# Optimization experiments

Hardware: AMD Instinct MI355X
Metric: run time of the kernel (lower is better)

## Reference

```python
import jax, jax.numpy as jnp
import numpy as np

B, N = 16, 4096
N_IN, E_OUT = 128, 128          # inpt_dim[1], outp_dim[0]
OUT_N = 128                     # outp_dim[1]
G_DIM, CTXT_DIM = 64, 64
NODE_IN = E_OUT + N_IN          # 256, pre_ln size
CTXT_IN = G_DIM + CTXT_DIM      # 128
HID_F, HID_A = 256, 128
N_HEADS = 4
HEAD_DIM = OUT_N // N_HEADS     # 32
LN_EPS = 1e-5


def _init_w(key, fan_in, fan_out):
    return jax.random.normal(key, (fan_in, fan_out), jnp.float32) / np.float32(np.sqrt(fan_in))


def setup_inputs() -> dict:
    key = jax.random.key(0)
    ks = jax.random.split(key, 10)
    nodes = jax.random.normal(ks[0], (B, N, N_IN), jnp.float32)
    pooled_edges = jax.random.normal(ks[1], (B, N, E_OUT), jnp.float32)
    # variable-length graphs: valid prefix per graph (at least half the nodes)
    lengths = jax.random.randint(ks[2], (B,), N // 2, N + 1)
    mask = jnp.arange(N)[None, :] < lengths[:, None]
    globs = jax.random.normal(ks[3], (B, G_DIM), jnp.float32)
    ctxt = jax.random.normal(ks[4], (B, CTXT_DIM), jnp.float32)
    return {
        "nodes": nodes,
        "pooled_edges": pooled_edges,
        "mask": mask,
        "globs": globs,
        "ctxt": ctxt,
        "ln_g": jnp.ones((NODE_IN,), jnp.float32),
        "ln_b": jnp.zeros((NODE_IN,), jnp.float32),
        "feat_w1": _init_w(ks[5], NODE_IN + CTXT_IN, HID_F),
        "feat_b1": jnp.zeros((HID_F,), jnp.float32),
        "feat_w2": _init_w(ks[6], HID_F, OUT_N),
        "feat_b2": jnp.zeros((OUT_N,), jnp.float32),
        "attn_w1": _init_w(ks[7], NODE_IN + CTXT_IN, HID_A),
        "attn_b1": jnp.zeros((HID_A,), jnp.float32),
        "attn_w2": _init_w(ks[8], HID_A, N_HEADS),
        "attn_b2": jnp.zeros((N_HEADS,), jnp.float32),
    }


def _mlp(x, w1, b1, w2, b2):
    # DenseNetwork: one hidden block with LeakyReLU ("lrlu"), linear output
    h = jax.nn.leaky_relu(x @ w1 + b1)
    return h @ w2 + b2


def reference(nodes, pooled_edges, mask, globs, ctxt, ln_g, ln_b,
              feat_w1, feat_b1, feat_w2, feat_b2,
              attn_w1, attn_b1, attn_w2, attn_b2):
    # nodes = cat([graph.nodes, pooled_edges]) -> pre-LayerNorm
    x = jnp.concatenate([nodes, pooled_edges], axis=-1)           # [B,N,256]
    mu = jnp.mean(x, axis=-1, keepdims=True)
    var = jnp.var(x, axis=-1, keepdims=True)
    x = (x - mu) * jax.lax.rsqrt(var + LN_EPS) * ln_g + ln_b

    # high-level context broadcast to every node
    hl = jnp.concatenate([globs, ctxt], axis=-1)                   # [B,128]
    hl = jnp.broadcast_to(hl[:, None, :], (x.shape[0], x.shape[1], hl.shape[-1]))
    xin = jnp.concatenate([x, hl], axis=-1)                        # [B,N,384]

    # attention net with -inf padding, softmax over node axis (dim=-2)
    logits = _mlp(xin, attn_w1, attn_b1, attn_w2, attn_b2)          # [B,N,H]
    logits = jnp.where(mask[..., None], logits, -jnp.inf)
    w = jax.nn.softmax(logits, axis=1) / np.float32(np.sqrt(OUT_N))
    w = jnp.where(mask[..., None], w, 0.0)

    # feature net with 0 padding + residual (same_size)
    feats = _mlp(xin, feat_w1, feat_b1, feat_w2, feat_b2)           # [B,N,128]
    feats = jnp.where(mask[..., None], feats, 0.0)
    new_nodes = feats + nodes

    # expand per-head weights across head_dim, flatten, weighted node pooling
    w_full = jnp.repeat(w, HEAD_DIM, axis=-1)                       # [B,N,128]
    pooled = jnp.sum(new_nodes * w_full, axis=1)                    # [B,128]
    return (new_nodes, pooled)
```

## Files before the change

### kernel.cpp

```cpp
#include <hip/hip_runtime.h>
#include <stdint.h>

typedef unsigned short u16;
typedef unsigned char  u8;
typedef unsigned int   u32;
typedef __attribute__((ext_vector_type(8))) short bf16x8;
typedef __attribute__((ext_vector_type(4))) float f32x4;

static __device__ __forceinline__ float bf2f(u32 u) {
    union { u32 i; float f; } x; x.i = u << 16; return x.f;
}
static __device__ __forceinline__ u16 f2bf(float f) {
    union { u32 i; float f; } x; x.f = f;
    return (u16)((x.i + 0x7fffu + ((x.i >> 16) & 1u)) >> 16);
}
static __device__ __forceinline__ u32 packbf(float a, float b) {
    return (u32)f2bf(a) | ((u32)f2bf(b) << 16);
}
static __device__ __forceinline__ float ldf(const void* p, int i, int isf32) {
    return isf32 ? ((const float*)p)[i] : bf2f(((const u16*)p)[i]);
}
static __device__ __forceinline__ bool mvalid(const void* mask, int g, int mi32) {
    return mi32 ? (((const int*)mask)[g] != 0) : (((const u8*)mask)[g] != 0);
}

#define NTOT 65536
#define SXLD 264
#define SHLD 136
#define BM   64

__global__ __launch_bounds__(256) void k0_prep(
    const void* __restrict__ feat_w1, const void* __restrict__ attn_w1,
    const void* __restrict__ feat_b1, const void* __restrict__ attn_b1,
    const void* __restrict__ feat_w2, const void* __restrict__ attn_w2,
    const void* __restrict__ globs, const void* __restrict__ ctxt,
    const void* __restrict__ ln_g,
    u16* __restrict__ W1t, u16* __restrict__ W2t, u16* __restrict__ aw2t,
    float* __restrict__ hlc)
{
    __shared__ u16 tile[64][66];
    __shared__ float hl[128];
    const int isf32 = (((const u32*)ln_g)[0] == 0x3F800000u);
    const int bid = blockIdx.x;
    const int t = threadIdx.x;

    if (bid < 24) {
        int jt = bid >> 2, kt = bid & 3;
        int j0 = jt * 64, k0 = kt * 64;
        int jj = t & 63, kq = t >> 6;
#pragma unroll
        for (int r = 0; r < 16; r++) {
            int kk = r * 4 + kq;
            int j = j0 + jj;
            float v = (j < 256) ? ldf(feat_w1, (k0 + kk) * 256 + j, isf32)
                                : ldf(attn_w1, (k0 + kk) * 128 + (j - 256), isf32);
            tile[kk][jj] = f2bf(v);
        }
        __syncthreads();
        int kk2 = t & 63, jq = t >> 6;
#pragma unroll
        for (int r = 0; r < 16; r++) {
            int jj2 = r * 4 + jq;
            W1t[(size_t)(j0 + jj2) * 256 + k0 + kk2] = tile[kk2][jj2];
        }
    } else if (bid < 32) {
        int id2 = bid - 24;
        int ct2 = id2 >> 2, kt = id2 & 3;
        int c0 = ct2 * 64, k0 = kt * 64;
        int cc = t & 63, kq = t >> 6;
#pragma unroll
        for (int r = 0; r < 16; r++) {
            int kk = r * 4 + kq;
            tile[kk][cc] = f2bf(ldf(feat_w2, (k0 + kk) * 128 + c0 + cc, isf32));
        }
        __syncthreads();
        int kk2 = t & 63, cq = t >> 6;
#pragma unroll
        for (int r = 0; r < 16; r++) {
            int cc2 = r * 4 + cq;
            W2t[(size_t)(c0 + cc2) * 256 + k0 + kk2] = tile[kk2][cc2];
        }
    } else if (bid == 32) {
#pragma unroll
        for (int i = 0; i < 8; i++) {
            int e = i * 256 + t;
            int n = e >> 7, k = e & 127;
            aw2t[e] = (n < 4) ? f2bf(ldf(attn_w2, k * 4 + n, isf32)) : (u16)0;
        }
    } else {
        int b = bid - 33;
        if (t < 64)       hl[t] = ldf(globs, b * 64 + t, isf32);
        else if (t < 128) hl[t] = ldf(ctxt, b * 64 + (t - 64), isf32);
        __syncthreads();
        {
            float s = ldf(feat_b1, t, isf32);
#pragma unroll 8
            for (int c = 0; c < 128; c++)
                s += hl[c] * ldf(feat_w1, (256 + c) * 256 + t, isf32);
            hlc[b * 384 + t] = s;
        }
        if (t < 128) {
            float s = ldf(attn_b1, t, isf32);
#pragma unroll 8
            for (int c = 0; c < 128; c++)
                s += hl[c] * ldf(attn_w1, (256 + c) * 128 + t, isf32);
            hlc[b * 384 + 256 + t] = s;
        }
    }
}

__global__ __launch_bounds__(256, 3) void k_mega(
    const void* __restrict__ nodes, const void* __restrict__ edges,
    const void* __restrict__ ln_g, const void* __restrict__ ln_b,
    const u16* __restrict__ W1t, const u16* __restrict__ W2t,
    const u16* __restrict__ aw2t, const float* __restrict__ hlc,
    const void* __restrict__ attn_b2, const void* __restrict__ feat_b2,
    const void* __restrict__ mask,
    float* __restrict__ logits, void* __restrict__ outp)
{
    __shared__ __align__(16) u16 sX[BM * SXLD];
    __shared__ __align__(16) u16 sH[BM * SHLD];
    __shared__ float sG[256], sBt[256];
    const int t = threadIdx.x;
    const int g0 = blockIdx.x * BM;
    const int b = g0 >> 12;
    const int isf32 = (((const u32*)ln_g)[0] == 0x3F800000u);
    const int mi32  = (((const u32*)mask)[0] == 1u);

    sG[t]  = ldf(ln_g, t, isf32);
    sBt[t] = ldf(ln_b, t, isf32);
    __syncthreads();

#pragma unroll
    for (int half = 0; half < 2; half++) {
        const int r = half * 32 + (t >> 3), q8 = t & 7;
        u32 pk[16];
#pragma unroll
        for (int j = 0; j < 4; j++) {
            int c = q8 + j * 8;
            if (isf32) {
                const float* src = (c < 16)
                    ? ((const float*)nodes + (size_t)(g0 + r) * 128 + c * 8)
                    : ((const float*)edges + (size_t)(g0 + r) * 128 + (c - 16) * 8);
                float4 v0 = ((const float4*)src)[0];
                float4 v1 = ((const float4*)src)[1];
                pk[4 * j]     = packbf(v0.x, v0.y);
                pk[4 * j + 1] = packbf(v0.z, v0.w);
                pk[4 * j + 2] = packbf(v1.x, v1.y);
                pk[4 * j + 3] = packbf(v1.z, v1.w);
            } else {
                const u16* src = (c < 16)
                    ? ((const u16*)nodes + (size_t)(g0 + r) * 128 + c * 8)
                    : ((const u16*)edges + (size_t)(g0 + r) * 128 + (c - 16) * 8);
                uint4 v = ((const uint4*)src)[0];
                pk[4 * j] = v.x; pk[4 * j + 1] = v.y;
                pk[4 * j + 2] = v.z; pk[4 * j + 3] = v.w;
            }
        }
        float s = 0.f, q = 0.f;
#pragma unroll
        for (int i = 0; i < 16; i++) {
            float lo = bf2f(pk[i] & 0xffffu), hi = bf2f(pk[i] >> 16);
            s += lo + hi; q += lo * lo + hi * hi;
        }
        s += __shfl_xor(s, 1, 64); s += __shfl_xor(s, 2, 64); s += __shfl_xor(s, 4, 64);
        q += __shfl_xor(q, 1, 64); q += __shfl_xor(q, 2, 64); q += __shfl_xor(q, 4, 64);
        float mu = s * (1.f / 256.f);
        float var = q * (1.f / 256.f) - mu * mu;
        float rs = rsqrtf(var + 1e-5f);
#pragma unroll
        for (int j = 0; j < 4; j++) {
            int c = q8 + j * 8;
            u32 ow[4];
#pragma unroll
            for (int k2 = 0; k2 < 4; k2++) {
                int col = c * 8 + k2 * 2;
                u32 w2 = pk[4 * j + k2];
                float y0 = (bf2f(w2 & 0xffffu) - mu) * rs * sG[col]     + sBt[col];
                float y1 = (bf2f(w2 >> 16)     - mu) * rs * sG[col + 1] + sBt[col + 1];
                ow[k2] = packbf(y0, y1);
            }
            *(uint4*)&sX[r * SXLD + c * 8] = make_uint4(ow[0], ow[1], ow[2], ow[3]);
        }
    }
    __syncthreads();

    const int w = t >> 6, l = t & 63;
    const int lr = l & 15, lq = l >> 4;

    f32x4 acc2[4][2];
#pragma unroll
    for (int rt = 0; rt < 4; rt++)
#pragma unroll
        for (int ct = 0; ct < 2; ct++) acc2[rt][ct] = (f32x4){0.f, 0.f, 0.f, 0.f};

    const int order[3] = {2, 0, 1};
#pragma unroll
    for (int oi = 0; oi < 3; oi++) {
        const int nt = order[oi];

        float hbv[2];
#pragma unroll
        for (int ct = 0; ct < 2; ct++)
            hbv[ct] = hlc[b * 384 + nt * 128 + w * 32 + ct * 16 + lr];

        f32x4 acc1[4][2];
#pragma unroll
        for (int rt = 0; rt < 4; rt++)
#pragma unroll
            for (int ct = 0; ct < 2; ct++) acc1[rt][ct] = (f32x4){0.f, 0.f, 0.f, 0.f};

        const u16* Wp = W1t + (size_t)(nt * 128 + w * 32 + lr) * 256;
#pragma unroll
        for (int kh = 0; kh < 2; kh++) {
            bf16x8 bW[4][2];
#pragma unroll
            for (int kk = 0; kk < 4; kk++)
#pragma unroll
                for (int ct = 0; ct < 2; ct++)
                    bW[kk][ct] = *(const bf16x8*)(Wp + ct * 16 * 256 + (kh * 4 + kk) * 32 + lq * 8);
#pragma unroll
            for (int kk = 0; kk < 4; kk++) {
                bf16x8 aF[4];
#pragma unroll
                for (int rt = 0; rt < 4; rt++)
                    aF[rt] = *(const bf16x8*)&sX[(rt * 16 + lr) * SXLD + ((kh * 4 + kk) * 4 + lq) * 8];
#pragma unroll
                for (int rt = 0; rt < 4; rt++)
#pragma unroll
                    for (int ct = 0; ct < 2; ct++)
                        acc1[rt][ct] = __builtin_amdgcn_mfma_f32_16x16x32_bf16(aF[rt], bW[kk][ct], acc1[rt][ct], 0, 0, 0);
            }
        }

        __syncthreads();
#pragma unroll
        for (int rt = 0; rt < 4; rt++)
#pragma unroll
            for (int ct = 0; ct < 2; ct++)
#pragma unroll
                for (int reg = 0; reg < 4; reg++) {
                    int row = rt * 16 + lq * 4 + reg;
                    int col = w * 32 + ct * 16 + lr;
                    float hv = acc1[rt][ct][reg] + hbv[ct];
                    hv = (hv >= 0.f) ? hv : 0.01f * hv;
                    sH[row * SHLD + col] = f2bf(hv);
                }
        __syncthreads();

        if (nt == 2) {
            f32x4 accL = (f32x4){0.f, 0.f, 0.f, 0.f};
#pragma unroll
            for (int kk = 0; kk < 4; kk++) {
                bf16x8 aF = *(const bf16x8*)&sH[(w * 16 + lr) * SHLD + (kk * 4 + lq) * 8];
                bf16x8 bF = *(const bf16x8*)(aw2t + lr * 128 + kk * 32 + lq * 8);
                accL = __builtin_amdgcn_mfma_f32_16x16x32_bf16(aF, bF, accL, 0, 0, 0);
            }
            if (lr < 4) {
                float bias = ldf(attn_b2, lr, isf32);
#pragma unroll
                for (int reg = 0; reg < 4; reg++) {
                    int row = g0 + w * 16 + lq * 4 + reg;
                    logits[(size_t)lr * NTOT + row] = accL[reg] + bias;
                }
            }
        } else {
            const u16* W2p = W2t + (size_t)(w * 32 + lr) * 256 + nt * 128;
            bf16x8 bW2[4][2];
#pragma unroll
            for (int kk = 0; kk < 4; kk++)
#pragma unroll
                for (int ct = 0; ct < 2; ct++)
                    bW2[kk][ct] = *(const bf16x8*)(W2p + ct * 16 * 256 + kk * 32 + lq * 8);
#pragma unroll
            for (int kk = 0; kk < 4; kk++) {
                bf16x8 aF[4];
#pragma unroll
                for (int rt = 0; rt < 4; rt++)
                    aF[rt] = *(const bf16x8*)&sH[(rt * 16 + lr) * SHLD + (kk * 4 + lq) * 8];
#pragma unroll
                for (int rt = 0; rt < 4; rt++)
#pragma unroll
                    for (int ct = 0; ct < 2; ct++)
                        acc2[rt][ct] = __builtin_amdgcn_mfma_f32_16x16x32_bf16(aF[rt], bW2[kk][ct], acc2[rt][ct], 0, 0, 0);
            }
        }
    }

#pragma unroll
    for (int rt = 0; rt < 4; rt++)
#pragma unroll
        for (int ct = 0; ct < 2; ct++)
#pragma unroll
            for (int reg = 0; reg < 4; reg++) {
                int row = rt * 16 + lq * 4 + reg;
                int col = w * 32 + ct * 16 + lr;
                int g = g0 + row;
                float v = acc2[rt][ct][reg] + ldf(feat_b2, col, isf32);
                v = mvalid(mask, g, mi32) ? v : 0.f;
                v += ldf(nodes, g * 128 + col, isf32);
                size_t idx = (size_t)g * 128 + col;
                if (isf32) ((float*)outp)[idx] = v;
                else       ((u16*)outp)[idx] = f2bf(v);
            }
}

__global__ __launch_bounds__(1024) void k_softmax(
    const float* __restrict__ logits, const void* __restrict__ mask,
    const void* __restrict__ ln_g,
    float* __restrict__ wbuf, float* __restrict__ pooled)
{
    __shared__ float red[32];
    const int bh = blockIdx.x;
    const int b = bh >> 2, h = bh & 3;
    const int t = threadIdx.x;
    const int mi32 = (((const u32*)mask)[0] == 1u);
    if (t < 32) pooled[bh * 32 + t] = 0.f;

    float4 lg = ((const float4*)(logits + (size_t)h * NTOT + b * 4096))[t];
    int v0, v1, v2, v3;
    if (mi32) {
        int4 m4 = ((const int4*)mask)[b * 1024 + t];
        v0 = m4.x; v1 = m4.y; v2 = m4.z; v3 = m4.w;
    } else {
        u32 mb = ((const u32*)mask)[b * 1024 + t];
        v0 = mb & 255; v1 = (mb >> 8) & 255; v2 = (mb >> 16) & 255; v3 = mb >> 24;
    }
    float mx = -1e30f;
    if (v0) mx = lg.x;
    if (v1) mx = fmaxf(mx, lg.y);
    if (v2) mx = fmaxf(mx, lg.z);
    if (v3) mx = fmaxf(mx, lg.w);
#pragma unroll
    for (int o = 1; o < 64; o <<= 1) mx = fmaxf(mx, __shfl_xor(mx, o, 64));
    if ((t & 63) == 0) red[t >> 6] = mx;
    __syncthreads();
    float m2 = red[0];
#pragma unroll
    for (int i = 1; i < 16; i++) m2 = fmaxf(m2, red[i]);
    float e0 = v0 ? expf(lg.x - m2) : 0.f;
    float e1 = v1 ? expf(lg.y - m2) : 0.f;
    float e2 = v2 ? expf(lg.z - m2) : 0.f;
    float e3 = v3 ? expf(lg.w - m2) : 0.f;
    float sv = e0 + e1 + e2 + e3;
#pragma unroll
    for (int o = 1; o < 64; o <<= 1) sv += __shfl_xor(sv, o, 64);
    __syncthreads();
    if ((t & 63) == 0) red[16 + (t >> 6)] = sv;
    __syncthreads();
    float s2 = 0.f;
#pragma unroll
    for (int i = 0; i < 16; i++) s2 += red[16 + i];
    float inv = 0.08838834764831845f / s2;
    float4 o4 = make_float4(e0 * inv, e1 * inv, e2 * inv, e3 * inv);
    ((float4*)(wbuf + (size_t)h * NTOT + b * 4096))[t] = o4;
}

__global__ __launch_bounds__(256) void k_pool(
    const void* __restrict__ outp, const float* __restrict__ wbuf,
    const void* __restrict__ ln_g, float* __restrict__ pooled)
{
    __shared__ float sW[4][32];
    __shared__ float pacc[8][128];
    const int blk = blockIdx.x;
    const int b = blk >> 7, s = blk & 127;
    const int t = threadIdx.x;
    const int isf32 = (((const u32*)ln_g)[0] == 0x3F800000u);

    if (t < 128) {
        int h = t >> 5, n = t & 31;
        sW[h][n] = wbuf[(size_t)h * NTOT + b * 4096 + s * 32 + n];
    }
    __syncthreads();

    const int c4 = (t & 31) * 4, r8 = t >> 5;
    const int h = c4 >> 5;
    const size_t rowbase = (size_t)(b * 4096 + s * 32);
    float a0 = 0.f, a1 = 0.f, a2 = 0.f, a3 = 0.f;
    if (isf32) {
        const float* op = (const float*)outp;
#pragma unroll
        for (int i = 0; i < 4; i++) {
            int row = i * 8 + r8;
            float4 v = *(const float4*)(op + (rowbase + row) * 128 + c4);
            float wv = sW[h][row];
            a0 += v.x * wv; a1 += v.y * wv; a2 += v.z * wv; a3 += v.w * wv;
        }
    } else {
        const u16* op = (const u16*)outp;
#pragma unroll
        for (int i = 0; i < 4; i++) {
            int row = i * 8 + r8;
            uint2 v = *(const uint2*)(op + (rowbase + row) * 128 + c4);
            float wv = sW[h][row];
            a0 += bf2f(v.x & 0xffffu) * wv; a1 += bf2f(v.x >> 16) * wv;
            a2 += bf2f(v.y & 0xffffu) * wv; a3 += bf2f(v.y >> 16) * wv;
        }
    }
    *(float4*)&pacc[r8][c4] = make_float4(a0, a1, a2, a3);
    __syncthreads();
    if (t < 128) {
        float sum = 0.f;
#pragma unroll
        for (int r = 0; r < 8; r++) sum += pacc[r][t];
        atomicAdd(&pooled[b * 128 + t], sum);
    }
}

__global__ __launch_bounds__(256) void k_fin(const float* __restrict__ pooled,
                                             const void* __restrict__ ln_g,
                                             void* __restrict__ outbase)
{
    int t = blockIdx.x * 256 + threadIdx.x;
    const int isf32 = (((const u32*)ln_g)[0] == 0x3F800000u);
    if (t < 2048) {
        size_t off = (size_t)NTOT * 128 + t;
        if (isf32) ((float*)outbase)[off] = pooled[t];
        else       ((u16*)outbase)[off] = f2bf(pooled[t]);
    }
}

extern "C" void kernel_launch(void* const* d_in, const int* in_sizes, int n_in,
                              void* d_out, int out_size, void* d_ws, size_t ws_size,
                              hipStream_t stream)
{
    const void* nodes   = d_in[0];
    const void* edges   = d_in[1];
    const void* mask    = d_in[2];
    const void* globs   = d_in[3];
    const void* ctxt    = d_in[4];
    const void* ln_g    = d_in[5];
    const void* ln_b    = d_in[6];
    const void* feat_w1 = d_in[7];
    const void* feat_b1 = d_in[8];
    const void* feat_w2 = d_in[9];
    const void* feat_b2 = d_in[10];
    const void* attn_w1 = d_in[11];
    const void* attn_b1 = d_in[12];
    const void* attn_w2 = d_in[13];
    const void* attn_b2 = d_in[14];

    char* ws = (char*)d_ws;
    u16*   W1t    = (u16*)ws;   ws += (size_t)384 * 256 * 2;
    u16*   W2t    = (u16*)ws;   ws += (size_t)128 * 256 * 2;
    u16*   aw2t   = (u16*)ws;   ws += (size_t)16 * 128 * 2;
    float* hlc    = (float*)ws; ws += (size_t)16 * 384 * 4;
    float* logits = (float*)ws; ws += (size_t)NTOT * 4 * 4;
    float* wbuf   = (float*)ws; ws += (size_t)NTOT * 4 * 4;
    float* pooled = (float*)ws; ws += (size_t)2048 * 4;

    k0_prep  <<<dim3(49),   dim3(256),  0, stream>>>(feat_w1, attn_w1, feat_b1, attn_b1,
                                                     feat_w2, attn_w2, globs, ctxt, ln_g,
                                                     W1t, W2t, aw2t, hlc);
    k_mega   <<<dim3(1024), dim3(256),  0, stream>>>(nodes, edges, ln_g, ln_b, W1t, W2t,
                                                     aw2t, hlc, attn_b2, feat_b2, mask,
                                                     logits, d_out);
    k_softmax<<<dim3(64),   dim3(1024), 0, stream>>>(logits, mask, ln_g, wbuf, pooled);
    k_pool   <<<dim3(2048), dim3(256),  0, stream>>>(d_out, wbuf, ln_g, pooled);
    k_fin    <<<dim3(8),    dim3(256),  0, stream>>>(pooled, ln_g, d_out);
}
```

Before: 229.0 us.

## Split mega-kernel tile into two 32-row subtiles with prefetch and double-buffered sH

Each block now processes its 64 rows as two sequential 32-row subtiles instead of one 64-row tile. The global loads for both subtiles are issued up front so the second tile's input fetch overlaps the first tile's compute. The hidden-activation buffer is double-buffered, which removes one barrier per stage, and occupancy is raised from 3 to 4 blocks per CU through the smaller LDS footprint and fewer accumulators. In exchange, W1/W2 weight fragments are reloaded for each subtile, and the registers holding the prefetched data add pressure.

```diff
diff --git a/kernel.cpp b/kernel.cpp
--- a/kernel.cpp
+++ b/kernel.cpp
@@ -27,7 +27,10 @@
 #define NTOT 65536
 #define SXLD 264
 #define SHLD 136
-#define BM   64
+
+#define BAR() do { asm volatile("s_waitcnt lgkmcnt(0)" ::: "memory"); \
+                   __builtin_amdgcn_s_barrier();                      \
+                   asm volatile("" ::: "memory"); } while (0)
 
 __global__ __launch_bounds__(256) void k0_prep(
     const void* __restrict__ feat_w1, const void* __restrict__ attn_w1,
@@ -109,7 +112,7 @@
     }
 }
 
-__global__ __launch_bounds__(256, 3) void k_mega(
+__global__ __launch_bounds__(256, 4) void k_mega(
     const void* __restrict__ nodes, const void* __restrict__ edges,
     const void* __restrict__ ln_g, const void* __restrict__ ln_b,
     const u16* __restrict__ W1t, const u16* __restrict__ W2t,
@@ -118,45 +121,62 @@
     const void* __restrict__ mask,
     float* __restrict__ logits, void* __restrict__ outp)
 {
-    __shared__ __align__(16) u16 sX[BM * SXLD];
-    __shared__ __align__(16) u16 sH[BM * SHLD];
+    __shared__ __align__(16) u16 sX[32 * SXLD];
+    __shared__ __align__(16) u16 sH[2][32 * SHLD];
     __shared__ float sG[256], sBt[256];
     const int t = threadIdx.x;
-    const int g0 = blockIdx.x * BM;
-    const int b = g0 >> 12;
     const int isf32 = (((const u32*)ln_g)[0] == 0x3F800000u);
     const int mi32  = (((const u32*)mask)[0] == 1u);
+    const int r = t >> 3, q8 = t & 7;
+    const int g00 = blockIdx.x * 64;
+    const int g01 = g00 + 32;
 
     sG[t]  = ldf(ln_g, t, isf32);
     sBt[t] = ldf(ln_b, t, isf32);
-    __syncthreads();
-
-#pragma unroll
-    for (int half = 0; half < 2; half++) {
-        const int r = half * 32 + (t >> 3), q8 = t & 7;
-        u32 pk[16];
+
+    float4 f0a[4], f0b[4], f1a[4];
+    uint4  u0[4],  u1[4];
+    if (isf32) {
 #pragma unroll
         for (int j = 0; j < 4; j++) {
             int c = q8 + j * 8;
-            if (isf32) {
-                const float* src = (c < 16)
-                    ? ((const float*)nodes + (size_t)(g0 + r) * 128 + c * 8)
-                    : ((const float*)edges + (size_t)(g0 + r) * 128 + (c - 16) * 8);
-                float4 v0 = ((const float4*)src)[0];
-                float4 v1 = ((const float4*)src)[1];
-                pk[4 * j]     = packbf(v0.x, v0.y);
-                pk[4 * j + 1] = packbf(v0.z, v0.w);
-                pk[4 * j + 2] = packbf(v1.x, v1.y);
-                pk[4 * j + 3] = packbf(v1.z, v1.w);
-            } else {
-                const u16* src = (c < 16)
-                    ? ((const u16*)nodes + (size_t)(g0 + r) * 128 + c * 8)
-                    : ((const u16*)edges + (size_t)(g0 + r) * 128 + (c - 16) * 8);
-                uint4 v = ((const uint4*)src)[0];
-                pk[4 * j] = v.x; pk[4 * j + 1] = v.y;
-                pk[4 * j + 2] = v.z; pk[4 * j + 3] = v.w;
-            }
-        }
+            const float* s0 = (c < 16)
+                ? ((const float*)nodes + (size_t)(g00 + r) * 128 + c * 8)
+                : ((const float*)edges + (size_t)(g00 + r) * 128 + (c - 16) * 8);
+            f0a[j] = ((const float4*)s0)[0];
+            f0b[j] = ((const float4*)s0)[1];
+        }
+#pragma unroll
+        for (int j = 0; j < 4; j++) {
+            int c = q8 + j * 8;
+            const float* s1 = (c < 16)
+                ? ((const float*)nodes + (size_t)(g01 + r) * 128 + c * 8)
+                : ((const float*)edges + (size_t)(g01 + r) * 128 + (c - 16) * 8);
+            f1a[j] = ((const float4*)s1)[0];
+        }
+    } else {
+#pragma unroll
+        for (int j = 0; j < 4; j++) {
+            int c = q8 + j * 8;
+            const u16* s0 = (c < 16)
+                ? ((const u16*)nodes + (size_t)(g00 + r) * 128 + c * 8)
+                : ((const u16*)edges + (size_t)(g00 + r) * 128 + (c - 16) * 8);
+            u0[j] = ((const uint4*)s0)[0];
+        }
+#pragma unroll
+        for (int j = 0; j < 4; j++) {
+            int c = q8 + j * 8;
+            const u16* s1 = (c < 16)
+                ? ((const u16*)nodes + (size_t)(g01 + r) * 128 + c * 8)
+                : ((const u16*)edges + (size_t)(g01 + r) * 128 + (c - 16) * 8);
+            u1[j] = ((const uint4*)s1)[0];
+        }
+    }
+    BAR();
+
+    u32 pk[16];
+
+    auto ln_to_sX = [&]() {
         float s = 0.f, q = 0.f;
 #pragma unroll
         for (int i = 0; i < 16; i++) {
@@ -182,127 +202,176 @@
             }
             *(uint4*)&sX[r * SXLD + c * 8] = make_uint4(ow[0], ow[1], ow[2], ow[3]);
         }
-    }
-    __syncthreads();
+    };
+
+    if (isf32) {
+#pragma unroll
+        for (int j = 0; j < 4; j++) {
+            pk[4 * j]     = packbf(f0a[j].x, f0a[j].y);
+            pk[4 * j + 1] = packbf(f0a[j].z, f0a[j].w);
+            pk[4 * j + 2] = packbf(f0b[j].x, f0b[j].y);
+            pk[4 * j + 3] = packbf(f0b[j].z, f0b[j].w);
+        }
+    } else {
+#pragma unroll
+        for (int j = 0; j < 4; j++) {
+            pk[4 * j] = u0[j].x; pk[4 * j + 1] = u0[j].y;
+            pk[4 * j + 2] = u0[j].z; pk[4 * j + 3] = u0[j].w;
+        }
+    }
+    ln_to_sX();
+    BAR();
 
     const int w = t >> 6, l = t & 63;
     const int lr = l & 15, lq = l >> 4;
 
-    f32x4 acc2[4][2];
-#pragma unroll
-    for (int rt = 0; rt < 4; rt++)
-#pragma unroll
-        for (int ct = 0; ct < 2; ct++) acc2[rt][ct] = (f32x4){0.f, 0.f, 0.f, 0.f};
-
-    const int order[3] = {2, 0, 1};
-#pragma unroll
-    for (int oi = 0; oi < 3; oi++) {
-        const int nt = order[oi];
-
-        float hbv[2];
-#pragma unroll
-        for (int ct = 0; ct < 2; ct++)
-            hbv[ct] = hlc[b * 384 + nt * 128 + w * 32 + ct * 16 + lr];
-
-        f32x4 acc1[4][2];
-#pragma unroll
-        for (int rt = 0; rt < 4; rt++)
-#pragma unroll
-            for (int ct = 0; ct < 2; ct++) acc1[rt][ct] = (f32x4){0.f, 0.f, 0.f, 0.f};
-
-        const u16* Wp = W1t + (size_t)(nt * 128 + w * 32 + lr) * 256;
-#pragma unroll
-        for (int kh = 0; kh < 2; kh++) {
-            bf16x8 bW[4][2];
-#pragma unroll
-            for (int kk = 0; kk < 4; kk++)
+    auto do_tile = [&](int g0) {
+        const int b = g0 >> 12;
+        f32x4 acc2[2][2];
+#pragma unroll
+        for (int rt = 0; rt < 2; rt++)
+#pragma unroll
+            for (int ct = 0; ct < 2; ct++) acc2[rt][ct] = (f32x4){0.f, 0.f, 0.f, 0.f};
+
+        const int order[3] = {2, 0, 1};
+#pragma unroll
+        for (int oi = 0; oi < 3; oi++) {
+            const int nt = order[oi];
+            u16* sHc = &sH[oi & 1][0];
+
+            float hbv[2];
+#pragma unroll
+            for (int ct = 0; ct < 2; ct++)
+                hbv[ct] = hlc[b * 384 + nt * 128 + w * 32 + ct * 16 + lr];
+
+            f32x4 acc1[2][2];
+#pragma unroll
+            for (int rt = 0; rt < 2; rt++)
+#pragma unroll
+                for (int ct = 0; ct < 2; ct++) acc1[rt][ct] = (f32x4){0.f, 0.f, 0.f, 0.f};
+
+            const u16* Wp = W1t + (size_t)(nt * 128 + w * 32 + lr) * 256;
+#pragma unroll
+            for (int kh = 0; kh < 2; kh++) {
+                bf16x8 bW[4][2];
+#pragma unroll
+                for (int kk = 0; kk < 4; kk++)
+#pragma unroll
+                    for (int ct = 0; ct < 2; ct++)
+                        bW[kk][ct] = *(const bf16x8*)(Wp + ct * 16 * 256 + (kh * 4 + kk) * 32 + lq * 8);
+#pragma unroll
+                for (int kk = 0; kk < 4; kk++) {
+                    bf16x8 aF[2];
+#pragma unroll
+                    for (int rt = 0; rt < 2; rt++)
+                        aF[rt] = *(const bf16x8*)&sX[(rt * 16 + lr) * SXLD + ((kh * 4 + kk) * 4 + lq) * 8];
+#pragma unroll
+                    for (int rt = 0; rt < 2; rt++)
+#pragma unroll
+                        for (int ct = 0; ct < 2; ct++)
+                            acc1[rt][ct] = __builtin_amdgcn_mfma_f32_16x16x32_bf16(aF[rt], bW[kk][ct], acc1[rt][ct], 0, 0, 0);
+                }
+            }
+
+#pragma unroll
+            for (int rt = 0; rt < 2; rt++)
 #pragma unroll
                 for (int ct = 0; ct < 2; ct++)
-                    bW[kk][ct] = *(const bf16x8*)(Wp + ct * 16 * 256 + (kh * 4 + kk) * 32 + lq * 8);
-#pragma unroll
-            for (int kk = 0; kk < 4; kk++) {
-                bf16x8 aF[4];
-#pragma unroll
-                for (int rt = 0; rt < 4; rt++)
-                    aF[rt] = *(const bf16x8*)&sX[(rt * 16 + lr) * SXLD + ((kh * 4 + kk) * 4 + lq) * 8];
-#pragma unroll
-                for (int rt = 0; rt < 4; rt++)
+#pragma unroll
+                    for (int reg = 0; reg < 4; reg++) {
+                        int row = rt * 16 + lq * 4 + reg;
+                        int col = w * 32 + ct * 16 + lr;
+                        float hv = acc1[rt][ct][reg] + hbv[ct];
+                        hv = (hv >= 0.f) ? hv : 0.01f * hv;
+                        sHc[row * SHLD + col] = f2bf(hv);
+                    }
+            BAR();
+
+            if (nt == 2) {
+                if (w < 2) {
+                    f32x4 accL = (f32x4){0.f, 0.f, 0.f, 0.f};
+#pragma unroll
+                    for (int kk = 0; kk < 4; kk++) {
+                        bf16x8 aF = *(const bf16x8*)&sHc[(w * 16 + lr) * SHLD + (kk * 4 + lq) * 8];
+                        bf16x8 bF = *(const bf16x8*)(aw2t + lr * 128 + kk * 32 + lq * 8);
+                        accL = __builtin_amdgcn_mfma_f32_16x16x32_bf16(aF, bF, accL, 0, 0, 0);
+                    }
+                    if (lr < 4) {
+                        float bias = ldf(attn_b2, lr, isf32);
+#pragma unroll
+                        for (int reg = 0; reg < 4; reg++) {
+                            int row = g0 + w * 16 + lq * 4 + reg;
+                            logits[(size_t)lr * NTOT + row] = accL[reg] + bias;
+                        }
+                    }
+                }
+            } else {
+                const u16* W2p = W2t + (size_t)(w * 32 + lr) * 256 + nt * 128;
+                bf16x8 bW2[4][2];
+#pragma unroll
+                for (int kk = 0; kk < 4; kk++)
 #pragma unroll
                     for (int ct = 0; ct < 2; ct++)
-                        acc1[rt][ct] = __builtin_amdgcn_mfma_f32_16x16x32_bf16(aF[rt], bW[kk][ct], acc1[rt][ct], 0, 0, 0);
+                        bW2[kk][ct] = *(const bf16x8*)(W2p + ct * 16 * 256 + kk * 32 + lq * 8);
+#pragma unroll
+                for (int kk = 0; kk < 4; kk++) {
+                    bf16x8 aF[2];
+#pragma unroll
+                    for (int rt = 0; rt < 2; rt++)
+                        aF[rt] = *(const bf16x8*)&sHc[(rt * 16 + lr) * SHLD + (kk * 4 + lq) * 8];
+#pragma unroll
+                    for (int rt = 0; rt < 2; rt++)
+#pragma unroll
+                        for (int ct = 0; ct < 2; ct++)
+                            acc2[rt][ct] = __builtin_amdgcn_mfma_f32_16x16x32_bf16(aF[rt], bW2[kk][ct], acc2[rt][ct], 0, 0, 0);
+                }
             }
         }
 
-        __syncthreads();
-#pragma unroll
-        for (int rt = 0; rt < 4; rt++)
+#pragma unroll
+        for (int rt = 0; rt < 2; rt++)
 #pragma unroll
             for (int ct = 0; ct < 2; ct++)
 #pragma unroll
                 for (int reg = 0; reg < 4; reg++) {
                     int row = rt * 16 + lq * 4 + reg;
                     int col = w * 32 + ct * 16 + lr;
-                    float hv = acc1[rt][ct][reg] + hbv[ct];
-                    hv = (hv >= 0.f) ? hv : 0.01f * hv;
-                    sH[row * SHLD + col] = f2bf(hv);
+                    int g = g0 + row;
+                    float v = acc2[rt][ct][reg] + ldf(feat_b2, col, isf32);
+                    v = mvalid(mask, g, mi32) ? v : 0.f;
+                    v += ldf(nodes, g * 128 + col, isf32);
+                    size_t idx = (size_t)g * 128 + col;
+                    if (isf32) ((float*)outp)[idx] = v;
+                    else       ((u16*)outp)[idx] = f2bf(v);
                 }
-        __syncthreads();
-
-        if (nt == 2) {
-            f32x4 accL = (f32x4){0.f, 0.f, 0.f, 0.f};
-#pragma unroll
-            for (int kk = 0; kk < 4; kk++) {
-                bf16x8 aF = *(const bf16x8*)&sH[(w * 16 + lr) * SHLD + (kk * 4 + lq) * 8];
-                bf16x8 bF = *(const bf16x8*)(aw2t + lr * 128 + kk * 32 + lq * 8);
-                accL = __builtin_amdgcn_mfma_f32_16x16x32_bf16(aF, bF, accL, 0, 0, 0);
-            }
-            if (lr < 4) {
-                float bias = ldf(attn_b2, lr, isf32);
-#pragma unroll
-                for (int reg = 0; reg < 4; reg++) {
-                    int row = g0 + w * 16 + lq * 4 + reg;
-                    logits[(size_t)lr * NTOT + row] = accL[reg] + bias;
-                }
-            }
-        } else {
-            const u16* W2p = W2t + (size_t)(w * 32 + lr) * 256 + nt * 128;
-            bf16x8 bW2[4][2];
-#pragma unroll
-            for (int kk = 0; kk < 4; kk++)
-#pragma unroll
-                for (int ct = 0; ct < 2; ct++)
-                    bW2[kk][ct] = *(const bf16x8*)(W2p + ct * 16 * 256 + kk * 32 + lq * 8);
-#pragma unroll
-            for (int kk = 0; kk < 4; kk++) {
-                bf16x8 aF[4];
-#pragma unroll
-                for (int rt = 0; rt < 4; rt++)
-                    aF[rt] = *(const bf16x8*)&sH[(rt * 16 + lr) * SHLD + (kk * 4 + lq) * 8];
-#pragma unroll
-                for (int rt = 0; rt < 4; rt++)
-#pragma unroll
-                    for (int ct = 0; ct < 2; ct++)
-                        acc2[rt][ct] = __builtin_amdgcn_mfma_f32_16x16x32_bf16(aF[rt], bW2[kk][ct], acc2[rt][ct], 0, 0, 0);
-            }
-        }
-    }
-
-#pragma unroll
-    for (int rt = 0; rt < 4; rt++)
-#pragma unroll
-        for (int ct = 0; ct < 2; ct++)
-#pragma unroll
-            for (int reg = 0; reg < 4; reg++) {
-                int row = rt * 16 + lq * 4 + reg;
-                int col = w * 32 + ct * 16 + lr;
-                int g = g0 + row;
-                float v = acc2[rt][ct][reg] + ldf(feat_b2, col, isf32);
-                v = mvalid(mask, g, mi32) ? v : 0.f;
-                v += ldf(nodes, g * 128 + col, isf32);
-                size_t idx = (size_t)g * 128 + col;
-                if (isf32) ((float*)outp)[idx] = v;
-                else       ((u16*)outp)[idx] = f2bf(v);
-            }
+    };
+
+    do_tile(g00);
+
+    if (isf32) {
+#pragma unroll
+        for (int j = 0; j < 4; j++) {
+            int c = q8 + j * 8;
+            const float* s1 = (c < 16)
+                ? ((const float*)nodes + (size_t)(g01 + r) * 128 + c * 8)
+                : ((const float*)edges + (size_t)(g01 + r) * 128 + (c - 16) * 8);
+            float4 fb = ((const float4*)s1)[1];
+            pk[4 * j]     = packbf(f1a[j].x, f1a[j].y);
+            pk[4 * j + 1] = packbf(f1a[j].z, f1a[j].w);
+            pk[4 * j + 2] = packbf(fb.x, fb.y);
+            pk[4 * j + 3] = packbf(fb.z, fb.w);
+        }
+    } else {
+#pragma unroll
+        for (int j = 0; j < 4; j++) {
+            pk[4 * j] = u1[j].x; pk[4 * j + 1] = u1[j].y;
+            pk[4 * j + 2] = u1[j].z; pk[4 * j + 3] = u1[j].w;
+        }
+    }
+    ln_to_sX();
+    BAR();
+
+    do_tile(g01);
 }
 
 __global__ __launch_bounds__(1024) void k_softmax(
```

Result: slower. 242.1 us (+5.7%).

## Fuse softmax and weighted pooling into main kernel via per-block online-softmax partials

Applied to the files above, without the earlier changes.

Each 64-row block now computes its local max and exp-sum of the attention logits and its exp-weighted partial pooled sums while the output tile is still in registers. It writes only a small per-block record, and a single small final kernel rescales and combines the records. This removes the logits and weights round-trips, the re-read of the full output tensor in the pooling kernel, the atomics and two launches. The LDS row padding is also changed (264 to 260, 136 to 132), which alters bank-conflict behaviour and may misalign 16-byte LDS accesses.

```diff
diff --git a/kernel.cpp b/kernel.cpp
--- a/kernel.cpp
+++ b/kernel.cpp
@@ -25,9 +25,9 @@
 }
 
 #define NTOT 65536
-#define SXLD 264
-#define SHLD 136
-#define BM   64
+#define SXLD 260
+#define SHLD 132
+#define PVLD 136
 
 __global__ __launch_bounds__(256) void k0_prep(
     const void* __restrict__ feat_w1, const void* __restrict__ attn_w1,
@@ -116,13 +116,14 @@
     const u16* __restrict__ aw2t, const float* __restrict__ hlc,
     const void* __restrict__ attn_b2, const void* __restrict__ feat_b2,
     const void* __restrict__ mask,
-    float* __restrict__ logits, void* __restrict__ outp)
+    float* __restrict__ pv, void* __restrict__ outp)
 {
-    __shared__ __align__(16) u16 sX[BM * SXLD];
-    __shared__ __align__(16) u16 sH[BM * SHLD];
+    __shared__ __align__(16) u16 sX[64 * SXLD];
+    __shared__ __align__(16) u16 sH[64 * SHLD];
     __shared__ float sG[256], sBt[256];
+    __shared__ float sL[64][4];
     const int t = threadIdx.x;
-    const int g0 = blockIdx.x * BM;
+    const int g0 = blockIdx.x * 64;
     const int b = g0 >> 12;
     const int isf32 = (((const u32*)ln_g)[0] == 0x3F800000u);
     const int mi32  = (((const u32*)mask)[0] == 1u);
@@ -187,6 +188,9 @@
 
     const int w = t >> 6, l = t & 63;
     const int lr = l & 15, lq = l >> 4;
+    const float ab2 = (lr < 4) ? ldf(attn_b2, lr, isf32) : 0.f;
+    const float fb2_0 = ldf(feat_b2, w * 32 + lr, isf32);
+    const float fb2_1 = ldf(feat_b2, w * 32 + 16 + lr, isf32);
 
     f32x4 acc2[4][2];
 #pragma unroll
@@ -257,12 +261,9 @@
                 accL = __builtin_amdgcn_mfma_f32_16x16x32_bf16(aF, bF, accL, 0, 0, 0);
             }
             if (lr < 4) {
-                float bias = ldf(attn_b2, lr, isf32);
-#pragma unroll
-                for (int reg = 0; reg < 4; reg++) {
-                    int row = g0 + w * 16 + lq * 4 + reg;
-                    logits[(size_t)lr * NTOT + row] = accL[reg] + bias;
-                }
+#pragma unroll
+                for (int reg = 0; reg < 4; reg++)
+                    sL[w * 16 + lq * 4 + reg][lr] = accL[reg] + ab2;
             }
         } else {
             const u16* W2p = W2t + (size_t)(w * 32 + lr) * 256 + nt * 128;
@@ -287,6 +288,43 @@
         }
     }
 
+    float* pvb = pv + (size_t)blockIdx.x * PVLD;
+    if (w == 0) {
+        const int row = l;
+        const bool vld = mvalid(mask, g0 + row, mi32);
+        float lg0 = sL[row][0], lg1 = sL[row][1], lg2 = sL[row][2], lg3 = sL[row][3];
+        float x0 = vld ? lg0 : -1e30f;
+        float x1 = vld ? lg1 : -1e30f;
+        float x2 = vld ? lg2 : -1e30f;
+        float x3 = vld ? lg3 : -1e30f;
+#pragma unroll
+        for (int o = 1; o < 64; o <<= 1) {
+            x0 = fmaxf(x0, __shfl_xor(x0, o, 64));
+            x1 = fmaxf(x1, __shfl_xor(x1, o, 64));
+            x2 = fmaxf(x2, __shfl_xor(x2, o, 64));
+            x3 = fmaxf(x3, __shfl_xor(x3, o, 64));
+        }
+        float e0 = vld ? expf(lg0 - x0) : 0.f;
+        float e1 = vld ? expf(lg1 - x1) : 0.f;
+        float e2 = vld ? expf(lg2 - x2) : 0.f;
+        float e3 = vld ? expf(lg3 - x3) : 0.f;
+        sL[row][0] = e0; sL[row][1] = e1; sL[row][2] = e2; sL[row][3] = e3;
+        float s0 = e0, s1 = e1, s2 = e2, s3 = e3;
+#pragma unroll
+        for (int o = 1; o < 64; o <<= 1) {
+            s0 += __shfl_xor(s0, o, 64);
+            s1 += __shfl_xor(s1, o, 64);
+            s2 += __shfl_xor(s2, o, 64);
+            s3 += __shfl_xor(s3, o, 64);
+        }
+        if (l == 0) {
+            pvb[128] = s0; pvb[129] = s1; pvb[130] = s2; pvb[131] = s3;
+            pvb[132] = x0; pvb[133] = x1; pvb[134] = x2; pvb[135] = x3;
+        }
+    }
+    __syncthreads();
+
+    float pc0 = 0.f, pc1 = 0.f;
 #pragma unroll
     for (int rt = 0; rt < 4; rt++)
 #pragma unroll
@@ -296,127 +334,75 @@
                 int row = rt * 16 + lq * 4 + reg;
                 int col = w * 32 + ct * 16 + lr;
                 int g = g0 + row;
-                float v = acc2[rt][ct][reg] + ldf(feat_b2, col, isf32);
+                float v = acc2[rt][ct][reg] + (ct ? fb2_1 : fb2_0);
                 v = mvalid(mask, g, mi32) ? v : 0.f;
                 v += ldf(nodes, g * 128 + col, isf32);
                 size_t idx = (size_t)g * 128 + col;
                 if (isf32) ((float*)outp)[idx] = v;
                 else       ((u16*)outp)[idx] = f2bf(v);
-            }
-}
-
-__global__ __launch_bounds__(1024) void k_softmax(
-    const float* __restrict__ logits, const void* __restrict__ mask,
-    const void* __restrict__ ln_g,
-    float* __restrict__ wbuf, float* __restrict__ pooled)
+                float e = sL[row][w];
+                if (ct) pc1 += e * v; else pc0 += e * v;
+            }
+    pc0 += __shfl_xor(pc0, 16, 64); pc0 += __shfl_xor(pc0, 32, 64);
+    pc1 += __shfl_xor(pc1, 16, 64); pc1 += __shfl_xor(pc1, 32, 64);
+    if (lq == 0) {
+        pvb[w * 32 + lr]      = pc0;
+        pvb[w * 32 + 16 + lr] = pc1;
+    }
+}
+
+__global__ __launch_bounds__(256) void k_final(
+    const float* __restrict__ pv, const void* __restrict__ ln_g,
+    void* __restrict__ outbase)
 {
-    __shared__ float red[32];
-    const int bh = blockIdx.x;
-    const int b = bh >> 2, h = bh & 3;
-    const int t = threadIdx.x;
-    const int mi32 = (((const u32*)mask)[0] == 1u);
-    if (t < 32) pooled[bh * 32 + t] = 0.f;
-
-    float4 lg = ((const float4*)(logits + (size_t)h * NTOT + b * 4096))[t];
-    int v0, v1, v2, v3;
-    if (mi32) {
-        int4 m4 = ((const int4*)mask)[b * 1024 + t];
-        v0 = m4.x; v1 = m4.y; v2 = m4.z; v3 = m4.w;
-    } else {
-        u32 mb = ((const u32*)mask)[b * 1024 + t];
-        v0 = mb & 255; v1 = (mb >> 8) & 255; v2 = (mb >> 16) & 255; v3 = mb >> 24;
-    }
-    float mx = -1e30f;
-    if (v0) mx = lg.x;
-    if (v1) mx = fmaxf(mx, lg.y);
-    if (v2) mx = fmaxf(mx, lg.z);
-    if (v3) mx = fmaxf(mx, lg.w);
-#pragma unroll
-    for (int o = 1; o < 64; o <<= 1) mx = fmaxf(mx, __shfl_xor(mx, o, 64));
-    if ((t & 63) == 0) red[t >> 6] = mx;
-    __syncthreads();
-    float m2 = red[0];
-#pragma unroll
-    for (int i = 1; i < 16; i++) m2 = fmaxf(m2, red[i]);
-    float e0 = v0 ? expf(lg.x - m2) : 0.f;
-    float e1 = v1 ? expf(lg.y - m2) : 0.f;
-    float e2 = v2 ? expf(lg.z - m2) : 0.f;
-    float e3 = v3 ? expf(lg.w - m2) : 0.f;
-    float sv = e0 + e1 + e2 + e3;
-#pragma unroll
-    for (int o = 1; o < 64; o <<= 1) sv += __shfl_xor(sv, o, 64);
-    __syncthreads();
-    if ((t & 63) == 0) red[16 + (t >> 6)] = sv;
-    __syncthreads();
-    float s2 = 0.f;
-#pragma unroll
-    for (int i = 0; i < 16; i++) s2 += red[16 + i];
-    float inv = 0.08838834764831845f / s2;
-    float4 o4 = make_float4(e0 * inv, e1 * inv, e2 * inv, e3 * inv);
-    ((float4*)(wbuf + (size_t)h * NTOT + b * 4096))[t] = o4;
-}
-
-__global__ __launch_bounds__(256) void k_pool(
-    const void* __restrict__ outp, const float* __restrict__ wbuf,
-    const void* __restrict__ ln_g, float* __restrict__ pooled)
-{
-    __shared__ float sW[4][32];
-    __shared__ float pacc[8][128];
-    const int blk = blockIdx.x;
-    const int b = blk >> 7, s = blk & 127;
+    __shared__ float sm[64][4], ss[64][4], se[64][4];
+    __shared__ float sZ[4];
+    __shared__ float part[2][128];
+    const int b = blockIdx.x;
     const int t = threadIdx.x;
     const int isf32 = (((const u32*)ln_g)[0] == 0x3F800000u);
-
+    const float* pvb = pv + (size_t)b * 64 * PVLD;
+
+#pragma unroll
+    for (int i = t; i < 512; i += 256) {
+        int rec = i >> 3, j = i & 7;
+        float x = pvb[(size_t)rec * PVLD + 128 + j];
+        if (j < 4) ss[rec][j] = x;
+        else       sm[rec][j - 4] = x;
+    }
+    __syncthreads();
+
+    {
+        const int h = t >> 6, i = t & 63;
+        float m = sm[i][h];
+#pragma unroll
+        for (int o = 1; o < 64; o <<= 1) m = fmaxf(m, __shfl_xor(m, o, 64));
+        float e = expf(sm[i][h] - m);
+        se[i][h] = e;
+        float z = e * ss[i][h];
+#pragma unroll
+        for (int o = 1; o < 64; o <<= 1) z += __shfl_xor(z, o, 64);
+        if (i == 0) sZ[h] = z;
+    }
+    __syncthreads();
+
+    {
+        const int c = t & 127, half = t >> 7;
+        const int h = c >> 5;
+        float acc = 0.f;
+#pragma unroll 8
+        for (int j = 0; j < 32; j++) {
+            int rec = half * 32 + j;
+            acc += se[rec][h] * pvb[(size_t)rec * PVLD + c];
+        }
+        part[half][c] = acc;
+    }
+    __syncthreads();
     if (t < 128) {
-        int h = t >> 5, n = t & 31;
-        sW[h][n] = wbuf[(size_t)h * NTOT + b * 4096 + s * 32 + n];
-    }
-    __syncthreads();
-
-    const int c4 = (t & 31) * 4, r8 = t >> 5;
-    const int h = c4 >> 5;
-    const size_t rowbase = (size_t)(b * 4096 + s * 32);
-    float a0 = 0.f, a1 = 0.f, a2 = 0.f, a3 = 0.f;
-    if (isf32) {
-        const float* op = (const float*)outp;
-#pragma unroll
-        for (int i = 0; i < 4; i++) {
-            int row = i * 8 + r8;
-            float4 v = *(const float4*)(op + (rowbase + row) * 128 + c4);
-            float wv = sW[h][row];
-            a0 += v.x * wv; a1 += v.y * wv; a2 += v.z * wv; a3 += v.w * wv;
-        }
-    } else {
-        const u16* op = (const u16*)outp;
-#pragma unroll
-        for (int i = 0; i < 4; i++) {
-            int row = i * 8 + r8;
-            uint2 v = *(const uint2*)(op + (rowbase + row) * 128 + c4);
-            float wv = sW[h][row];
-            a0 += bf2f(v.x & 0xffffu) * wv; a1 += bf2f(v.x >> 16) * wv;
-            a2 += bf2f(v.y & 0xffffu) * wv; a3 += bf2f(v.y >> 16) * wv;
-        }
-    }
-    *(float4*)&pacc[r8][c4] = make_float4(a0, a1, a2, a3);
-    __syncthreads();
-    if (t < 128) {
-        float sum = 0.f;
-#pragma unroll
-        for (int r = 0; r < 8; r++) sum += pacc[r][t];
-        atomicAdd(&pooled[b * 128 + t], sum);
-    }
-}
-
-__global__ __launch_bounds__(256) void k_fin(const float* __restrict__ pooled,
-                                             const void* __restrict__ ln_g,
-                                             void* __restrict__ outbase)
-{
-    int t = blockIdx.x * 256 + threadIdx.x;
-    const int isf32 = (((const u32*)ln_g)[0] == 0x3F800000u);
-    if (t < 2048) {
-        size_t off = (size_t)NTOT * 128 + t;
-        if (isf32) ((float*)outbase)[off] = pooled[t];
-        else       ((u16*)outbase)[off] = f2bf(pooled[t]);
+        float p = (part[0][t] + part[1][t]) * (0.08838834764831845f / sZ[t >> 5]);
+        size_t off = (size_t)NTOT * 128 + (size_t)b * 128 + t;
+        if (isf32) ((float*)outbase)[off] = p;
+        else       ((u16*)outbase)[off] = f2bf(p);
     }
 }
 
@@ -445,17 +431,13 @@
     u16*   W2t    = (u16*)ws;   ws += (size_t)128 * 256 * 2;
     u16*   aw2t   = (u16*)ws;   ws += (size_t)16 * 128 * 2;
     float* hlc    = (float*)ws; ws += (size_t)16 * 384 * 4;
-    float* logits = (float*)ws; ws += (size_t)NTOT * 4 * 4;
-    float* wbuf   = (float*)ws; ws += (size_t)NTOT * 4 * 4;
-    float* pooled = (float*)ws; ws += (size_t)2048 * 4;
-
-    k0_prep  <<<dim3(49),   dim3(256),  0, stream>>>(feat_w1, attn_w1, feat_b1, attn_b1,
-                                                     feat_w2, attn_w2, globs, ctxt, ln_g,
-                                                     W1t, W2t, aw2t, hlc);
-    k_mega   <<<dim3(1024), dim3(256),  0, stream>>>(nodes, edges, ln_g, ln_b, W1t, W2t,
-                                                     aw2t, hlc, attn_b2, feat_b2, mask,
-                                                     logits, d_out);
-    k_softmax<<<dim3(64),   dim3(1024), 0, stream>>>(logits, mask, ln_g, wbuf, pooled);
-    k_pool   <<<dim3(2048), dim3(256),  0, stream>>>(d_out, wbuf, ln_g, pooled);
-    k_fin    <<<dim3(8),    dim3(256),  0, stream>>>(pooled, ln_g, d_out);
-}
+    float* pv     = (float*)ws; ws += (size_t)1024 * PVLD * 4;
+
+    k0_prep <<<dim3(49),   dim3(256), 0, stream>>>(feat_w1, attn_w1, feat_b1, attn_b1,
+                                                   feat_w2, attn_w2, globs, ctxt, ln_g,
+                                                   W1t, W2t, aw2t, hlc);
+    k_mega  <<<dim3(1024), dim3(256), 0, stream>>>(nodes, edges, ln_g, ln_b, W1t, W2t,
+                                                   aw2t, hlc, attn_b2, feat_b2, mask,
+                                                   pv, d_out);
+    k_final <<<dim3(16),   dim3(256), 0, stream>>>(pv, ln_g, d_out);
+}
```

After: 220.1 us. -3.9%, faster.
